# Kernel tuning notes

Hardware: AMD Instinct MI355X
Metric: run time of the kernel (lower is better)

## Reference

```python
import jax, jax.numpy as jnp
import numpy as np

B, Q, KV, D, H = 2, 2048, 2048, 1024, 16
HD = D // H  # head dim = 64


def setup_inputs() -> dict:
    key = jax.random.key(0)
    ks = jax.random.split(key, 16)
    s = 1.0 / np.sqrt(D)
    return {
        "q": jax.random.normal(ks[0], (B, Q, D), jnp.float32),
        "k": jax.random.normal(ks[1], (B, KV, D), jnp.float32),
        "v": jax.random.normal(ks[2], (B, KV, D), jnp.float32),
        "past_k": jax.random.normal(ks[3], (B, KV, D), jnp.float32),
        "past_v": jax.random.normal(ks[4], (B, KV, D), jnp.float32),
        "mask": jax.random.randint(ks[5], (B, Q, KV + KV), 0, 2).astype(bool),
        "Wq": jax.random.uniform(ks[6], (D, D), jnp.float32, -s, s),
        "bq": jax.random.uniform(ks[7], (D,), jnp.float32, -s, s),
        "Wk": jax.random.uniform(ks[8], (D, D), jnp.float32, -s, s),
        "bk": jax.random.uniform(ks[9], (D,), jnp.float32, -s, s),
        "Wv": jax.random.uniform(ks[10], (D, D), jnp.float32, -s, s),
        "bv": jax.random.uniform(ks[11], (D,), jnp.float32, -s, s),
        "Wl": jax.random.uniform(ks[12], (D, D), jnp.float32, -s, s),
        "bl": jax.random.uniform(ks[13], (D,), jnp.float32, -s, s),
    }


def _split_heads(x):
    # (B, S, D) -> (B, H, S, HD)
    b, s, _ = x.shape
    return x.reshape(b, s, H, HD).transpose(0, 2, 1, 3)


def reference(q, k, v, past_k, past_v, mask, Wq, bq, Wk, bk, Wv, bv, Wl, bl):
    qp = q @ Wq.T + bq
    kp = k @ Wk.T + bk
    vp = v @ Wv.T + bv
    k_cat = jnp.concatenate([past_k, kp], axis=-2)  # (B, P+KV, D)
    v_cat = jnp.concatenate([past_v, vp], axis=-2)
    qh = _split_heads(qp)        # (B, H, Q, HD)
    kh = _split_heads(k_cat)     # (B, H, P+KV, HD)
    vh = _split_heads(v_cat)
    scores = jnp.einsum("bhqd,bhkd->bhqk", qh, kh) / np.sqrt(HD)
    scores = scores + mask[:, None].astype(scores.dtype) * (-10000.0)
    attn = jax.nn.softmax(scores, axis=-1)
    out = jnp.einsum("bhqk,bhkd->bhqd", attn, vh)  # (B, H, Q, HD)
    out = out.transpose(0, 2, 1, 3).reshape(q.shape[0], q.shape[1], D)
    x = out @ Wl.T + bl
    return (x, k_cat, v_cat)
```

## Files before the change

### kernel.cpp

```cpp
#include <hip/hip_runtime.h>

#define QLEN 2048
#define KVTOT 4096
#define DMODEL 1024
#define MASKC2 -14427.0f
#define SENT2  -28854.0f

typedef __attribute__((ext_vector_type(8))) short bf16x8;
typedef __attribute__((ext_vector_type(4))) float f32x4;
typedef unsigned short u16;
typedef unsigned int u32;
typedef unsigned long long u64;

__device__ __forceinline__ u16 f2b(float f) {
  union { float f; unsigned u; } v; v.f = f;
  unsigned r = v.u + 0x7FFFu + ((v.u >> 16) & 1u);
  return (u16)(r >> 16);
}

__device__ __forceinline__ float b2f(u16 x) {
  union { u32 u; float f; } v; v.u = (u32)x << 16; return v.f;
}

__device__ __forceinline__ u32 cvt_pk_bf16(float lo, float hi) {
  u32 r;
  asm("v_cvt_pk_bf16_f32 %0, %1, %2" : "=v"(r) : "v"(lo), "v"(hi));
  return r;
}

__device__ __forceinline__ float exp2v(float x) {
  float r;
  asm("v_exp_f32 %0, %1" : "=v"(r) : "v"(x));
  return r;
}

__device__ __forceinline__ float max3f(float a, float b, float c) {
  float r;
  asm("v_max3_f32 %0, %1, %2, %3" : "=v"(r) : "v"(a), "v"(b), "v"(c));
  return r;
}

__device__ __forceinline__ void gll16(const u16* g, u16* l) {
  __builtin_amdgcn_global_load_lds(
      (const __attribute__((address_space(1))) u32*)g,
      (__attribute__((address_space(3))) u32*)l, 16, 0, 0);
}

__global__ __launch_bounds__(256) void copy_past(
    const float* __restrict__ pk, const float* __restrict__ pv,
    float* __restrict__ kcat, float* __restrict__ vcat,
    u16* __restrict__ kh) {
  int i = blockIdx.x * 256 + threadIdx.x;
  int b = i >> 19;
  int r = i & 524287;
  size_t src = (size_t)i * 4;
  size_t dst = ((size_t)b * 1048576 + r) * 4;
  float4 kk = *(const float4*)&pk[src];
  float4 vv = *(const float4*)&pv[src];
  *(float4*)&kcat[dst] = kk;
  *(float4*)&vcat[dst] = vv;
  int s = r >> 8;
  int c4 = (r & 255) * 4;
  int h = c4 >> 6, d = c4 & 63;
  uint2 w = make_uint2(cvt_pk_bf16(kk.x, kk.y), cvt_pk_bf16(kk.z, kk.w));
  *(uint2*)&kh[((size_t)(b * 16 + h) * KVTOT + s) * 64 + d] = w;
}

__global__ __launch_bounds__(256) void maskpack(
    const int* __restrict__ mask, u64* __restrict__ bits) {
  int w = blockIdx.x * 4 + (threadIdx.x >> 6);
  int lane = threadIdx.x & 63;
  int mv = mask[(size_t)w * 64 + lane];
  u64 b = __ballot(mv != 0);
  if (lane == 0) bits[w] = b;
}

__global__ __launch_bounds__(256) void w2b(
    const float* __restrict__ w0, const float* __restrict__ w1,
    const float* __restrict__ w2, const float* __restrict__ w3,
    u16* __restrict__ dst) {
  const float* src = blockIdx.y == 0 ? w0 : blockIdx.y == 1 ? w1
                   : blockIdx.y == 2 ? w2 : w3;
  size_t i = ((size_t)blockIdx.x * 256 + threadIdx.x) * 8;
  float4 a = *(const float4*)&src[i];
  float4 b = *(const float4*)&src[i + 4];
  uint4 o = {cvt_pk_bf16(a.x, a.y), cvt_pk_bf16(a.z, a.w),
             cvt_pk_bf16(b.x, b.y), cvt_pk_bf16(b.z, b.w)};
  *(uint4*)&dst[(size_t)blockIdx.y * 1048576 + i] = o;
}

__global__ __launch_bounds__(256) void a2b(
    const float* __restrict__ a0, const float* __restrict__ a1,
    const float* __restrict__ a2, u16* __restrict__ dst0,
    u16* __restrict__ dst12) {
  const int y = blockIdx.y;
  const float* src = y == 0 ? a0 : y == 1 ? a1 : a2;
  u16* dst = y == 0 ? dst0 : dst12 + (size_t)(y - 1) * 4194304;
  size_t i = ((size_t)blockIdx.x * 256 + threadIdx.x) * 8;
  float4 a = *(const float4*)&src[i];
  float4 b = *(const float4*)&src[i + 4];
  uint4 o = {cvt_pk_bf16(a.x, a.y), cvt_pk_bf16(a.z, a.w),
             cvt_pk_bf16(b.x, b.y), cvt_pk_bf16(b.z, b.w)};
  *(uint4*)&dst[i] = o;
}

__global__ __launch_bounds__(256) void gemm_qkv(
    const u16* __restrict__ Ab0, const u16* __restrict__ Ab12,
    const u16* __restrict__ Wb,
    const float* __restrict__ bq, const float* __restrict__ bk,
    const float* __restrict__ bv,
    u16* __restrict__ qh, float* __restrict__ kcat, u16* __restrict__ kh,
    float* __restrict__ vcat) {
  const int K = 1024, N = 1024;
  __shared__ u16 As[128][32];
  __shared__ u16 Bs[128][32];
  const int z = blockIdx.z;
  const u16* A = (z == 0) ? Ab0 : Ab12 + (size_t)(z - 1) * 4194304;
  const u16* W = Wb + (size_t)z * 1048576;
  const float* bias = (z == 0) ? bq : (z == 1) ? bk : bv;
  const int t = threadIdx.x;
  const int m0 = blockIdx.y * 128, n0 = blockIdx.x * 128;
  const int lane = t & 63, wid = t >> 6;
  const int wr = (wid >> 1) * 64, wc = (wid & 1) * 64;
  const int lr = lane & 15, lg = lane >> 4;
  const int ko = lg * 8;

  f32x4 acc[4][4];
  #pragma unroll
  for (int m = 0; m < 4; ++m)
    #pragma unroll
    for (int n = 0; n < 4; ++n)
      acc[m][n] = (f32x4){0.f, 0.f, 0.f, 0.f};

  for (int k0 = 0; k0 < K; k0 += 32) {
    __syncthreads();
    #pragma unroll
    for (int j = 0; j < 2; ++j) {
      int idx = t + j * 256;
      int r = idx >> 2, c8 = (idx & 3) * 8;
      size_t ldsoff = (size_t)(j * 256 + (t & ~63)) * 8;
      gll16(A + (size_t)(m0 + r) * K + k0 + c8, &As[0][0] + ldsoff);
      gll16(W + (size_t)(n0 + r) * K + k0 + c8, &Bs[0][0] + ldsoff);
    }
    __syncthreads();
    bf16x8 av[4], bv4[4];
    #pragma unroll
    for (int m = 0; m < 4; ++m)
      av[m] = *(const bf16x8*)&As[wr + m * 16 + lr][ko];
    #pragma unroll
    for (int n = 0; n < 4; ++n)
      bv4[n] = *(const bf16x8*)&Bs[wc + n * 16 + lr][ko];
    #pragma unroll
    for (int m = 0; m < 4; ++m)
      #pragma unroll
      for (int n = 0; n < 4; ++n)
        acc[m][n] = __builtin_amdgcn_mfma_f32_16x16x32_bf16(av[m], bv4[n], acc[m][n], 0, 0, 0);
  }

  const int rq = lg * 4;
  #pragma unroll
  for (int m = 0; m < 4; ++m) {
    #pragma unroll
    for (int r = 0; r < 4; ++r) {
      int row = m0 + wr + m * 16 + rq + r;
      int bb = row >> 11, s = row & 2047;
      #pragma unroll
      for (int n = 0; n < 4; ++n) {
        int col = n0 + wc + n * 16 + lr;
        float val = acc[m][n][r] + bias[col];
        int hh = col >> 6, d = col & 63;
        if (z == 0) {
          qh[((size_t)(bb * 16 + hh) * QLEN + s) * 64 + d] = f2b(val * 0.18033688f);
        } else if (z == 1) {
          kcat[(size_t)(bb * 4096 + 2048 + s) * 1024 + col] = val;
          kh[((size_t)(bb * 16 + hh) * KVTOT + 2048 + s) * 64 + d] = f2b(val);
        } else {
          vcat[(size_t)(bb * 4096 + 2048 + s) * 1024 + col] = val;
        }
      }
    }
  }
}

__global__ __launch_bounds__(256) void gemm_out(
    const u16* __restrict__ A, const u16* __restrict__ W,
    const float* __restrict__ bias, float* __restrict__ C) {
  const int K = 1024, N = 1024;
  __shared__ u16 As[128][32];
  __shared__ u16 Bs[128][32];
  const int t = threadIdx.x;
  const int m0 = blockIdx.y * 128, n0 = blockIdx.x * 128;
  const int lane = t & 63, wid = t >> 6;
  const int wr = (wid >> 1) * 64, wc = (wid & 1) * 64;
  const int lr = lane & 15, lg = lane >> 4;
  const int ko = lg * 8;

  f32x4 acc[4][4];
  #pragma unroll
  for (int m = 0; m < 4; ++m)
    #pragma unroll
    for (int n = 0; n < 4; ++n)
      acc[m][n] = (f32x4){0.f, 0.f, 0.f, 0.f};

  for (int k0 = 0; k0 < K; k0 += 32) {
    __syncthreads();
    #pragma unroll
    for (int j = 0; j < 2; ++j) {
      int idx = t + j * 256;
      int r = idx >> 2, c8 = (idx & 3) * 8;
      size_t ldsoff = (size_t)(j * 256 + (t & ~63)) * 8;
      gll16(A + (size_t)(m0 + r) * K + k0 + c8, &As[0][0] + ldsoff);
      gll16(W + (size_t)(n0 + r) * K + k0 + c8, &Bs[0][0] + ldsoff);
    }
    __syncthreads();
    bf16x8 av[4], bv4[4];
    #pragma unroll
    for (int m = 0; m < 4; ++m)
      av[m] = *(const bf16x8*)&As[wr + m * 16 + lr][ko];
    #pragma unroll
    for (int n = 0; n < 4; ++n)
      bv4[n] = *(const bf16x8*)&Bs[wc + n * 16 + lr][ko];
    #pragma unroll
    for (int m = 0; m < 4; ++m)
      #pragma unroll
      for (int n = 0; n < 4; ++n)
        acc[m][n] = __builtin_amdgcn_mfma_f32_16x16x32_bf16(av[m], bv4[n], acc[m][n], 0, 0, 0);
  }

  const int rq = lg * 4;
  #pragma unroll
  for (int m = 0; m < 4; ++m) {
    #pragma unroll
    for (int r = 0; r < 4; ++r) {
      int row = m0 + wr + m * 16 + rq + r;
      float* cp = C + (size_t)row * N;
      #pragma unroll
      for (int n = 0; n < 4; ++n) {
        int col = n0 + wc + n * 16 + lr;
        cp[col] = acc[m][n][r] + bias[col];
      }
    }
  }
}

__global__ __launch_bounds__(256) void repack_vt(
    const float* __restrict__ src, u16* __restrict__ dst) {
  __shared__ u16 T[64][72];
  const int t = threadIdx.x;
  const int kv0 = blockIdx.x * 64;
  const int bh = blockIdx.y;
  const int b = bh >> 4, h = bh & 15;
  #pragma unroll
  for (int it = 0; it < 4; ++it) {
    int idx = t + it * 256;
    int r = idx >> 4;
    int c4 = (idx & 15) * 4;
    float4 v = *(const float4*)(src + (size_t)(b * KVTOT + kv0 + r) * DMODEL + h * 64 + c4);
    *(uint2*)&T[r][c4] = make_uint2(cvt_pk_bf16(v.x, v.y), cvt_pk_bf16(v.z, v.w));
  }
  __syncthreads();
  #pragma unroll
  for (int it = 0; it < 2; ++it) {
    int idx = t + it * 256;
    int d = idx & 63;
    int kc8 = (idx >> 6) * 8;
    bf16x8 o;
    #pragma unroll
    for (int j = 0; j < 8; ++j) o[j] = (short)T[kc8 + j][d];
    *(bf16x8*)(dst + (size_t)((b * 16 + h) * 64 + d) * KVTOT + kv0 + kc8) = o;
  }
}

__global__ __launch_bounds__(256, 2) void attn_mfma(
    const u16* __restrict__ qh, const u16* __restrict__ kh,
    const u16* __restrict__ vt, const u64* __restrict__ mbits,
    u16* __restrict__ out) {
  __shared__ __align__(16) u16 shm[4 * 64 * 72];
  __shared__ float mM[4][64];
  __shared__ float mL[4][64];
  const int t = threadIdx.x;
  const int wid = t >> 6, lane = t & 63;
  const int lr = lane & 15, lg = lane >> 4;
  const int fid = blockIdx.x;
  const int virt = (fid & 7) * 128 + (fid >> 3);
  const int bh = virt >> 5, qt = virt & 31;
  const int b = bh >> 4, h = bh & 15;
  const int q0 = qt * 64;

  u16* bufA = shm + wid * 2304;
  u16* bufB = bufA + 1152;

  bf16x8 ones;
  #pragma unroll
  for (int j = 0; j < 8; ++j) ones[j] = (short)0x3F80;

  bf16x8 qf[4][2];
  #pragma unroll
  for (int i = 0; i < 4; ++i) {
    const u16* qp = qh + ((size_t)bh * QLEN + q0 + i * 16 + lr) * 64 + lg * 8;
    qf[i][0] = *(const bf16x8*)qp;
    qf[i][1] = *(const bf16x8*)(qp + 32);
  }

  const u16* kbase = kh + (size_t)bh * KVTOT * 64 + (size_t)wid * 1024 * 64;
  const u16* vbase = vt + (size_t)bh * 64 * KVTOT + wid * 1024;
  const u64* mbase = mbits + ((size_t)b * QLEN + q0 + lr) * 64 + wid * 16;

  float mprev[4] = {SENT2, SENT2, SENT2, SENT2};
  f32x4 oacc[4][4];
  f32x4 oaccL[4];
  #pragma unroll
  for (int i = 0; i < 4; ++i) {
    oaccL[i] = (f32x4){0.f, 0.f, 0.f, 0.f};
    #pragma unroll
    for (int dt = 0; dt < 4; ++dt) oacc[i][dt] = (f32x4){0.f, 0.f, 0.f, 0.f};
  }

  bf16x8 kf[4][2];
  #pragma unroll
  for (int tile = 0; tile < 4; ++tile) {
    const u16* kp = kbase + (size_t)(tile * 16 + lr) * 64 + lg * 8;
    kf[tile][0] = *(const bf16x8*)kp;
    kf[tile][1] = *(const bf16x8*)(kp + 32);
  }

  auto QK = [&](int i, f32x4* sacc, u64 mb) {
    u64 mq = mb >> (lg * 4);
    const float negm = -mprev[i], negmm = MASKC2 - mprev[i];
    #pragma unroll
    for (int tile = 0; tile < 4; ++tile) {
      unsigned nib = (unsigned)((mq >> (tile * 16)) & 0xFull);
      #pragma unroll
      for (int r = 0; r < 4; ++r)
        sacc[tile][r] = (nib & (1u << r)) ? negmm : negm;
    }
    __builtin_amdgcn_s_setprio(1);
    #pragma unroll
    for (int tile = 0; tile < 4; ++tile) {
      sacc[tile] = __builtin_amdgcn_mfma_f32_16x16x32_bf16(kf[tile][0], qf[i][0], sacc[tile], 0, 0, 0);
      sacc[tile] = __builtin_amdgcn_mfma_f32_16x16x32_bf16(kf[tile][1], qf[i][1], sacc[tile], 0, 0, 0);
    }
    __builtin_amdgcn_s_setprio(0);
  };

  auto SM = [&](int i, f32x4* sacc, u16* pbuf) {
    float t1 = max3f(sacc[0][0], sacc[0][1], sacc[0][2]);
    float t2 = max3f(sacc[0][3], sacc[1][0], sacc[1][1]);
    float t3 = max3f(sacc[1][2], sacc[1][3], sacc[2][0]);
    float t4 = max3f(sacc[2][1], sacc[2][2], sacc[2][3]);
    float t5 = max3f(sacc[3][0], sacc[3][1], sacc[3][2]);
    float lmax = fmaxf(sacc[3][3], t1);
    lmax = max3f(lmax, t2, t3);
    lmax = max3f(lmax, t4, t5);
    if (!__all(lmax <= 11.0f)) {
      float rmax = fmaxf(lmax, __shfl_xor(lmax, 16));
      rmax = fmaxf(rmax, __shfl_xor(rmax, 32));
      float shift = fmaxf(rmax, 0.f);
      float corr = exp2v(-shift);
      float cr[4];
      #pragma unroll
      for (int r = 0; r < 4; ++r) cr[r] = __shfl(corr, lg * 4 + r);
      #pragma unroll
      for (int dt = 0; dt < 4; ++dt)
        #pragma unroll
        for (int r = 0; r < 4; ++r) oacc[i][dt][r] *= cr[r];
      #pragma unroll
      for (int r = 0; r < 4; ++r) oaccL[i][r] *= cr[r];
      mprev[i] += shift;
      #pragma unroll
      for (int tile = 0; tile < 4; ++tile)
        #pragma unroll
        for (int r = 0; r < 4; ++r) sacc[tile][r] -= shift;
    }
    #pragma unroll
    for (int tile = 0; tile < 4; ++tile) {
      float p0 = exp2v(sacc[tile][0]);
      float p1 = exp2v(sacc[tile][1]);
      float p2 = exp2v(sacc[tile][2]);
      float p3 = exp2v(sacc[tile][3]);
      *(uint2*)&pbuf[lr * 72 + tile * 16 + lg * 4] =
          make_uint2(cvt_pk_bf16(p0, p1), cvt_pk_bf16(p2, p3));
    }
  };

  f32x4 sA[4], sB[4];

  bf16x8 vf0[4][2], vf1[4][2];
  u64 mb0[4], mb1[4];

  #pragma unroll
  for (int i = 0; i < 4; ++i) mb0[i] = mbase[(size_t)i * 1024];
  #pragma unroll
  for (int dt = 0; dt < 4; ++dt) {
    const u16* vq = vbase + (size_t)(dt * 16 + lr) * KVTOT + lg * 8;
    vf0[dt][0] = *(const bf16x8*)vq;
    vf0[dt][1] = *(const bf16x8*)(vq + 32);
  }

#define PV_M(i, pbuf, VV)                                                      \
  {                                                                            \
    bf16x8 pa0 = *(const bf16x8*)&pbuf[lr * 72 + lg * 8];                      \
    bf16x8 pa1 = *(const bf16x8*)&pbuf[lr * 72 + 32 + lg * 8];                 \
    __builtin_amdgcn_s_setprio(1);                                             \
    _Pragma("unroll")                                                          \
    for (int dt = 0; dt < 4; ++dt) {                                           \
      oacc[i][dt] = __builtin_amdgcn_mfma_f32_16x16x32_bf16(pa0, VV[dt][0], oacc[i][dt], 0, 0, 0); \
      oacc[i][dt] = __builtin_amdgcn_mfma_f32_16x16x32_bf16(pa1, VV[dt][1], oacc[i][dt], 0, 0, 0); \
    }                                                                          \
    oaccL[i] = __builtin_amdgcn_mfma_f32_16x16x32_bf16(pa0, ones, oaccL[i], 0, 0, 0); \
    oaccL[i] = __builtin_amdgcn_mfma_f32_16x16x32_bf16(pa1, ones, oaccL[i], 0, 0, 0); \
    __builtin_amdgcn_s_setprio(0);                                             \
  }

#define ITER_M(IT, VCUR, VNXT, MCUR, MNXT)                                     \
  {                                                                            \
    const int it_ = (IT);                                                      \
    if (it_ + 1 < 16) {                                                        \
                     \
      _Pragma("unroll")                                                        \
      for (int i = 0; i < 4; ++i) MNXT[i] = mbase[(size_t)i * 1024 + it_ + 1]; \
      const u16* vp_ = vbase + (it_ + 1) * 64;                                 \
      _Pragma("unroll")                                                        \
      for (int dt = 0; dt < 4; ++dt) {                                         \
        const u16* vq_ = vp_ + (size_t)(dt * 16 + lr) * KVTOT + lg * 8;        \
        VNXT[dt][0] = *(const bf16x8*)vq_;                                     \
        VNXT[dt][1] = *(const bf16x8*)(vq_ + 32);                              \
      }                                                                        \
    }                                                                          \
    QK(0, sA, MCUR[0]);                                                        \
    SM(0, sA, bufA);                                                           \
    QK(1, sB, MCUR[1]);                                                        \
    PV_M(0, bufA, VCUR);                                                       \
    SM(1, sB, bufB);                                                           \
    QK(2, sA, MCUR[2]);                                                        \
    PV_M(1, bufB, VCUR);                                                       \
    SM(2, sA, bufA);                                                           \
    QK(3, sB, MCUR[3]);                                                        \
    if (it_ + 1 < 16) {                                                        \
      const u16* kp_ = kbase + (size_t)(it_ + 1) * 4096;                       \
      _Pragma("unroll")                                                        \
      for (int tile = 0; tile < 4; ++tile) {                                   \
        const u16* kq_ = kp_ + (size_t)(tile * 16 + lr) * 64 + lg * 8;         \
        kf[tile][0] = *(const bf16x8*)kq_;                                     \
        kf[tile][1] = *(const bf16x8*)(kq_ + 32);                              \
      }                                                                        \
    }                                                                          \
    PV_M(2, bufA, VCUR);                                                       \
    SM(3, sB, bufB);                                                           \
    PV_M(3, bufB, VCUR);                                                       \
  }

  for (int ii = 0; ii < 8; ++ii) {
    ITER_M(2 * ii,     vf0, vf1, mb0, mb1);
    ITER_M(2 * ii + 1, vf1, vf0, mb1, mb0);
  }
#undef ITER_M
#undef PV_M

  __syncthreads();
  u16* mo = shm + wid * 4608;
  #pragma unroll
  for (int i = 0; i < 4; ++i)
    #pragma unroll
    for (int dt = 0; dt < 4; ++dt)
      #pragma unroll
      for (int r = 0; r < 4; ++r)
        mo[(i * 16 + lg * 4 + r) * 72 + dt * 16 + lr] = f2b(oacc[i][dt][r]);
  if (lr == 0) {
    #pragma unroll
    for (int i = 0; i < 4; ++i)
      #pragma unroll
      for (int r = 0; r < 4; ++r)
        mL[wid][i * 16 + lg * 4 + r] = oaccL[i][r];
  }
  if (lg == 0) {
    #pragma unroll
    for (int i = 0; i < 4; ++i) mM[wid][i * 16 + lr] = mprev[i];
  }
  __syncthreads();

  const int q = wid * 16 + lr;
  float m0 = mM[0][q], m1 = mM[1][q], m2 = mM[2][q], m3 = mM[3][q];
  float mm = fmaxf(max3f(m0, m1, m2), m3);
  float w0 = exp2v(m0 - mm), w1 = exp2v(m1 - mm);
  float w2 = exp2v(m2 - mm), w3 = exp2v(m3 - mm);
  float l = mL[0][q] * w0 + mL[1][q] * w1 + mL[2][q] * w2 + mL[3][q] * w3;
  float inv = 1.f / l;
  float wgt[4] = {w0 * inv, w1 * inv, w2 * inv, w3 * inv};
  float o[16];
  #pragma unroll
  for (int j = 0; j < 16; ++j) o[j] = 0.f;
  #pragma unroll
  for (int w = 0; w < 4; ++w) {
    const u16* src = shm + w * 4608 + q * 72 + lg * 16;
    bf16x8 a0 = *(const bf16x8*)src;
    bf16x8 a1 = *(const bf16x8*)(src + 8);
    #pragma unroll
    for (int j = 0; j < 8; ++j) {
      o[j]     += b2f((u16)a0[j]) * wgt[w];
      o[8 + j] += b2f((u16)a1[j]) * wgt[w];
    }
  }
  u16* op = out + ((size_t)b * QLEN + q0 + q) * DMODEL + h * 64 + lg * 16;
  uint4 wA = {cvt_pk_bf16(o[0], o[1]), cvt_pk_bf16(o[2], o[3]),
              cvt_pk_bf16(o[4], o[5]), cvt_pk_bf16(o[6], o[7])};
  uint4 wB = {cvt_pk_bf16(o[8], o[9]), cvt_pk_bf16(o[10], o[11]),
              cvt_pk_bf16(o[12], o[13]), cvt_pk_bf16(o[14], o[15])};
  *(uint4*)op = wA;
  *(uint4*)(op + 8) = wB;
}

extern "C" void kernel_launch(void* const* d_in, const int* in_sizes, int n_in,
                              void* d_out, int out_size, void* d_ws, size_t ws_size,
                              hipStream_t stream) {
  const float* q      = (const float*)d_in[0];
  const float* k      = (const float*)d_in[1];
  const float* v      = (const float*)d_in[2];
  const float* past_k = (const float*)d_in[3];
  const float* past_v = (const float*)d_in[4];
  const int*   mask   = (const int*)d_in[5];
  const float* Wq     = (const float*)d_in[6];
  const float* bq     = (const float*)d_in[7];
  const float* Wk     = (const float*)d_in[8];
  const float* bk     = (const float*)d_in[9];
  const float* Wv     = (const float*)d_in[10];
  const float* bv     = (const float*)d_in[11];
  const float* Wl     = (const float*)d_in[12];
  const float* bl     = (const float*)d_in[13];

  float* xout = (float*)d_out;
  float* kcat = xout + 4194304;
  float* vcat = xout + 12582912;

  u16* wsb = (u16*)d_ws;
  u16* attno = wsb;
  u16* qh = wsb + 4194304;
  u16* kh = wsb + 8388608;
  u16* vt = wsb + 16777216;
  u16* Wb = wsb + 25165824;
  u64* mbits = (u64*)(wsb + 29360128);

  copy_past<<<4096, 256, 0, stream>>>(past_k, past_v, kcat, vcat, kh);
  maskpack<<<65536, 256, 0, stream>>>(mask, mbits);
  w2b<<<dim3(512, 4), 256, 0, stream>>>(Wq, Wk, Wv, Wl, Wb);
  a2b<<<dim3(2048, 3), 256, 0, stream>>>(q, k, v, attno, vt);

  gemm_qkv<<<dim3(8, 32, 3), 256, 0, stream>>>(
      attno, vt, Wb, bq, bk, bv, qh, kcat, kh, vcat);

  repack_vt<<<dim3(64, 32), 256, 0, stream>>>(vcat, vt);

  attn_mfma<<<1024, 256, 0, stream>>>(qh, kh, vt, mbits, attno);

  gemm_out<<<dim3(8, 32), 256, 0, stream>>>(attno, Wb + 3145728, bl, xout);
}
```

Before: 356.9 us.

## Merge prep conversion kernels into one launch and drop V register double-buffering

Folds the copy_past, w2b and a2b kernels into a single prep kernel that dispatches on block index, removing two kernel launches and their gaps. In the attention kernel, the V fragments are no longer prefetched one iteration ahead into a second register set; they are loaded at the start of each iteration into a single buffer. This lowers VGPR pressure and may raise occupancy, but exposes V load latency to the first PV step of each iteration. Also renames a local variable in the GEMMs to avoid clashing with the new av parameter.

```diff
diff --git a/kernel.cpp b/kernel.cpp
--- a/kernel.cpp
+++ b/kernel.cpp
@@ -46,24 +46,54 @@
       (__attribute__((address_space(3))) u32*)l, 16, 0, 0);
 }
 
-__global__ __launch_bounds__(256) void copy_past(
+__global__ __launch_bounds__(256) void prep(
     const float* __restrict__ pk, const float* __restrict__ pv,
     float* __restrict__ kcat, float* __restrict__ vcat,
-    u16* __restrict__ kh) {
-  int i = blockIdx.x * 256 + threadIdx.x;
-  int b = i >> 19;
-  int r = i & 524287;
-  size_t src = (size_t)i * 4;
-  size_t dst = ((size_t)b * 1048576 + r) * 4;
-  float4 kk = *(const float4*)&pk[src];
-  float4 vv = *(const float4*)&pv[src];
-  *(float4*)&kcat[dst] = kk;
-  *(float4*)&vcat[dst] = vv;
-  int s = r >> 8;
-  int c4 = (r & 255) * 4;
-  int h = c4 >> 6, d = c4 & 63;
-  uint2 w = make_uint2(cvt_pk_bf16(kk.x, kk.y), cvt_pk_bf16(kk.z, kk.w));
-  *(uint2*)&kh[((size_t)(b * 16 + h) * KVTOT + s) * 64 + d] = w;
+    u16* __restrict__ kh,
+    const float* __restrict__ w0, const float* __restrict__ w1,
+    const float* __restrict__ w2, const float* __restrict__ w3,
+    u16* __restrict__ wdst,
+    const float* __restrict__ aq, const float* __restrict__ ak,
+    const float* __restrict__ av, u16* __restrict__ adst0,
+    u16* __restrict__ adst12) {
+  const int bid = blockIdx.x;
+  if (bid < 4096) {
+    int i = bid * 256 + threadIdx.x;
+    int b = i >> 19;
+    int r = i & 524287;
+    size_t src = (size_t)i * 4;
+    size_t dst = ((size_t)b * 1048576 + r) * 4;
+    float4 kk = *(const float4*)&pk[src];
+    float4 vv = *(const float4*)&pv[src];
+    *(float4*)&kcat[dst] = kk;
+    *(float4*)&vcat[dst] = vv;
+    int s = r >> 8;
+    int c4 = (r & 255) * 4;
+    int h = c4 >> 6, d = c4 & 63;
+    uint2 w = make_uint2(cvt_pk_bf16(kk.x, kk.y), cvt_pk_bf16(kk.z, kk.w));
+    *(uint2*)&kh[((size_t)(b * 16 + h) * KVTOT + s) * 64 + d] = w;
+  } else if (bid < 6144) {
+    int t2 = bid - 4096;
+    int y = t2 >> 9, x = t2 & 511;
+    const float* src = y == 0 ? w0 : y == 1 ? w1 : y == 2 ? w2 : w3;
+    size_t i = ((size_t)x * 256 + threadIdx.x) * 8;
+    float4 a = *(const float4*)&src[i];
+    float4 b = *(const float4*)&src[i + 4];
+    uint4 o = {cvt_pk_bf16(a.x, a.y), cvt_pk_bf16(a.z, a.w),
+               cvt_pk_bf16(b.x, b.y), cvt_pk_bf16(b.z, b.w)};
+    *(uint4*)&wdst[(size_t)y * 1048576 + i] = o;
+  } else {
+    int t3 = bid - 6144;
+    int y = t3 >> 11, x = t3 & 2047;
+    const float* src = y == 0 ? aq : y == 1 ? ak : av;
+    u16* dst = y == 0 ? adst0 : adst12 + (size_t)(y - 1) * 4194304;
+    size_t i = ((size_t)x * 256 + threadIdx.x) * 8;
+    float4 a = *(const float4*)&src[i];
+    float4 b = *(const float4*)&src[i + 4];
+    uint4 o = {cvt_pk_bf16(a.x, a.y), cvt_pk_bf16(a.z, a.w),
+               cvt_pk_bf16(b.x, b.y), cvt_pk_bf16(b.z, b.w)};
+    *(uint4*)&dst[i] = o;
+  }
 }
 
 __global__ __launch_bounds__(256) void maskpack(
@@ -73,35 +103,6 @@
   int mv = mask[(size_t)w * 64 + lane];
   u64 b = __ballot(mv != 0);
   if (lane == 0) bits[w] = b;
-}
-
-__global__ __launch_bounds__(256) void w2b(
-    const float* __restrict__ w0, const float* __restrict__ w1,
-    const float* __restrict__ w2, const float* __restrict__ w3,
-    u16* __restrict__ dst) {
-  const float* src = blockIdx.y == 0 ? w0 : blockIdx.y == 1 ? w1
-                   : blockIdx.y == 2 ? w2 : w3;
-  size_t i = ((size_t)blockIdx.x * 256 + threadIdx.x) * 8;
-  float4 a = *(const float4*)&src[i];
-  float4 b = *(const float4*)&src[i + 4];
-  uint4 o = {cvt_pk_bf16(a.x, a.y), cvt_pk_bf16(a.z, a.w),
-             cvt_pk_bf16(b.x, b.y), cvt_pk_bf16(b.z, b.w)};
-  *(uint4*)&dst[(size_t)blockIdx.y * 1048576 + i] = o;
-}
-
-__global__ __launch_bounds__(256) void a2b(
-    const float* __restrict__ a0, const float* __restrict__ a1,
-    const float* __restrict__ a2, u16* __restrict__ dst0,
-    u16* __restrict__ dst12) {
-  const int y = blockIdx.y;
-  const float* src = y == 0 ? a0 : y == 1 ? a1 : a2;
-  u16* dst = y == 0 ? dst0 : dst12 + (size_t)(y - 1) * 4194304;
-  size_t i = ((size_t)blockIdx.x * 256 + threadIdx.x) * 8;
-  float4 a = *(const float4*)&src[i];
-  float4 b = *(const float4*)&src[i + 4];
-  uint4 o = {cvt_pk_bf16(a.x, a.y), cvt_pk_bf16(a.z, a.w),
-             cvt_pk_bf16(b.x, b.y), cvt_pk_bf16(b.z, b.w)};
-  *(uint4*)&dst[i] = o;
 }
 
 __global__ __launch_bounds__(256) void gemm_qkv(
@@ -143,10 +144,10 @@
       gll16(W + (size_t)(n0 + r) * K + k0 + c8, &Bs[0][0] + ldsoff);
     }
     __syncthreads();
-    bf16x8 av[4], bv4[4];
+    bf16x8 av4[4], bv4[4];
     #pragma unroll
     for (int m = 0; m < 4; ++m)
-      av[m] = *(const bf16x8*)&As[wr + m * 16 + lr][ko];
+      av4[m] = *(const bf16x8*)&As[wr + m * 16 + lr][ko];
     #pragma unroll
     for (int n = 0; n < 4; ++n)
       bv4[n] = *(const bf16x8*)&Bs[wc + n * 16 + lr][ko];
@@ -154,7 +155,7 @@
     for (int m = 0; m < 4; ++m)
       #pragma unroll
       for (int n = 0; n < 4; ++n)
-        acc[m][n] = __builtin_amdgcn_mfma_f32_16x16x32_bf16(av[m], bv4[n], acc[m][n], 0, 0, 0);
+        acc[m][n] = __builtin_amdgcn_mfma_f32_16x16x32_bf16(av4[m], bv4[n], acc[m][n], 0, 0, 0);
   }
 
   const int rq = lg * 4;
@@ -213,10 +214,10 @@
       gll16(W + (size_t)(n0 + r) * K + k0 + c8, &Bs[0][0] + ldsoff);
     }
     __syncthreads();
-    bf16x8 av[4], bv4[4];
+    bf16x8 av4[4], bv4[4];
     #pragma unroll
     for (int m = 0; m < 4; ++m)
-      av[m] = *(const bf16x8*)&As[wr + m * 16 + lr][ko];
+      av4[m] = *(const bf16x8*)&As[wr + m * 16 + lr][ko];
     #pragma unroll
     for (int n = 0; n < 4; ++n)
       bv4[n] = *(const bf16x8*)&Bs[wc + n * 16 + lr][ko];
@@ -224,7 +225,7 @@
     for (int m = 0; m < 4; ++m)
       #pragma unroll
       for (int n = 0; n < 4; ++n)
-        acc[m][n] = __builtin_amdgcn_mfma_f32_16x16x32_bf16(av[m], bv4[n], acc[m][n], 0, 0, 0);
+        acc[m][n] = __builtin_amdgcn_mfma_f32_16x16x32_bf16(av4[m], bv4[n], acc[m][n], 0, 0, 0);
   }
 
   const int rq = lg * 4;
@@ -324,6 +325,8 @@
     kf[tile][1] = *(const bf16x8*)(kp + 32);
   }
 
+  bf16x8 vf[4][2];
+
   auto QK = [&](int i, f32x4* sacc, u64 mb) {
     u64 mq = mb >> (lg * 4);
     const float negm = -mprev[i], negmm = MASKC2 - mprev[i];
@@ -383,57 +386,49 @@
     }
   };
 
+  auto PV = [&](int i, const u16* pbuf) {
+    bf16x8 pa0 = *(const bf16x8*)&pbuf[lr * 72 + lg * 8];
+    bf16x8 pa1 = *(const bf16x8*)&pbuf[lr * 72 + 32 + lg * 8];
+    __builtin_amdgcn_s_setprio(1);
+    #pragma unroll
+    for (int dt = 0; dt < 4; ++dt) {
+      oacc[i][dt] = __builtin_amdgcn_mfma_f32_16x16x32_bf16(pa0, vf[dt][0], oacc[i][dt], 0, 0, 0);
+      oacc[i][dt] = __builtin_amdgcn_mfma_f32_16x16x32_bf16(pa1, vf[dt][1], oacc[i][dt], 0, 0, 0);
+    }
+    oaccL[i] = __builtin_amdgcn_mfma_f32_16x16x32_bf16(pa0, ones, oaccL[i], 0, 0, 0);
+    oaccL[i] = __builtin_amdgcn_mfma_f32_16x16x32_bf16(pa1, ones, oaccL[i], 0, 0, 0);
+    __builtin_amdgcn_s_setprio(0);
+  };
+
   f32x4 sA[4], sB[4];
 
-  bf16x8 vf0[4][2], vf1[4][2];
   u64 mb0[4], mb1[4];
-
   #pragma unroll
   for (int i = 0; i < 4; ++i) mb0[i] = mbase[(size_t)i * 1024];
-  #pragma unroll
-  for (int dt = 0; dt < 4; ++dt) {
-    const u16* vq = vbase + (size_t)(dt * 16 + lr) * KVTOT + lg * 8;
-    vf0[dt][0] = *(const bf16x8*)vq;
-    vf0[dt][1] = *(const bf16x8*)(vq + 32);
-  }
-
-#define PV_M(i, pbuf, VV)                                                      \
+
+#define ITER_M(IT, MCUR, MNXT)                                                 \
   {                                                                            \
-    bf16x8 pa0 = *(const bf16x8*)&pbuf[lr * 72 + lg * 8];                      \
-    bf16x8 pa1 = *(const bf16x8*)&pbuf[lr * 72 + 32 + lg * 8];                 \
-    __builtin_amdgcn_s_setprio(1);                                             \
+    const int it_ = (IT);                                                      \
+                         \
+    const u16* vp_ = vbase + it_ * 64;                                         \
     _Pragma("unroll")                                                          \
     for (int dt = 0; dt < 4; ++dt) {                                           \
-      oacc[i][dt] = __builtin_amdgcn_mfma_f32_16x16x32_bf16(pa0, VV[dt][0], oacc[i][dt], 0, 0, 0); \
-      oacc[i][dt] = __builtin_amdgcn_mfma_f32_16x16x32_bf16(pa1, VV[dt][1], oacc[i][dt], 0, 0, 0); \
+      const u16* vq_ = vp_ + (size_t)(dt * 16 + lr) * KVTOT + lg * 8;          \
+      vf[dt][0] = *(const bf16x8*)vq_;                                         \
+      vf[dt][1] = *(const bf16x8*)(vq_ + 32);                                  \
     }                                                                          \
-    oaccL[i] = __builtin_amdgcn_mfma_f32_16x16x32_bf16(pa0, ones, oaccL[i], 0, 0, 0); \
-    oaccL[i] = __builtin_amdgcn_mfma_f32_16x16x32_bf16(pa1, ones, oaccL[i], 0, 0, 0); \
-    __builtin_amdgcn_s_setprio(0);                                             \
-  }
-
-#define ITER_M(IT, VCUR, VNXT, MCUR, MNXT)                                     \
-  {                                                                            \
-    const int it_ = (IT);                                                      \
+                \
     if (it_ + 1 < 16) {                                                        \
-                     \
       _Pragma("unroll")                                                        \
       for (int i = 0; i < 4; ++i) MNXT[i] = mbase[(size_t)i * 1024 + it_ + 1]; \
-      const u16* vp_ = vbase + (it_ + 1) * 64;                                 \
-      _Pragma("unroll")                                                        \
-      for (int dt = 0; dt < 4; ++dt) {                                         \
-        const u16* vq_ = vp_ + (size_t)(dt * 16 + lr) * KVTOT + lg * 8;        \
-        VNXT[dt][0] = *(const bf16x8*)vq_;                                     \
-        VNXT[dt][1] = *(const bf16x8*)(vq_ + 32);                              \
-      }                                                                        \
     }                                                                          \
     QK(0, sA, MCUR[0]);                                                        \
     SM(0, sA, bufA);                                                           \
     QK(1, sB, MCUR[1]);                                                        \
-    PV_M(0, bufA, VCUR);                                                       \
+    PV(0, bufA);                                                               \
     SM(1, sB, bufB);                                                           \
     QK(2, sA, MCUR[2]);                                                        \
-    PV_M(1, bufB, VCUR);                                                       \
+    PV(1, bufB);                                                               \
     SM(2, sA, bufA);                                                           \
     QK(3, sB, MCUR[3]);                                                        \
     if (it_ + 1 < 16) {                                                        \
@@ -445,17 +440,16 @@
         kf[tile][1] = *(const bf16x8*)(kq_ + 32);                              \
       }                                                                        \
     }                                                                          \
-    PV_M(2, bufA, VCUR);                                                       \
+    PV(2, bufA);                                                               \
     SM(3, sB, bufB);                                                           \
-    PV_M(3, bufB, VCUR);                                                       \
+    PV(3, bufB);                                                               \
   }
 
   for (int ii = 0; ii < 8; ++ii) {
-    ITER_M(2 * ii,     vf0, vf1, mb0, mb1);
-    ITER_M(2 * ii + 1, vf1, vf0, mb1, mb0);
+    ITER_M(2 * ii,     mb0, mb1);
+    ITER_M(2 * ii + 1, mb1, mb0);
   }
 #undef ITER_M
-#undef PV_M
 
   __syncthreads();
   u16* mo = shm + wid * 4608;
@@ -540,10 +534,10 @@
   u16* Wb = wsb + 25165824;
   u64* mbits = (u64*)(wsb + 29360128);
 
-  copy_past<<<4096, 256, 0, stream>>>(past_k, past_v, kcat, vcat, kh);
   maskpack<<<65536, 256, 0, stream>>>(mask, mbits);
-  w2b<<<dim3(512, 4), 256, 0, stream>>>(Wq, Wk, Wv, Wl, Wb);
-  a2b<<<dim3(2048, 3), 256, 0, stream>>>(q, k, v, attno, vt);
+  prep<<<12288, 256, 0, stream>>>(past_k, past_v, kcat, vcat, kh,
+                                  Wq, Wk, Wv, Wl, Wb,
+                                  q, k, v, attno, vt);
 
   gemm_qkv<<<dim3(8, 32, 3), 256, 0, stream>>>(
       attno, vt, Wb, bq, bk, bv, qh, kcat, kh, vcat);
```

Result: faster. 295.4 us (-17.2%).
